# Kernel optimization log

Measured on AMD Instinct MI355X. Metric: run time of the kernel, lower is better.

Reference implementation:

```python
import jax, jax.numpy as jnp
import numpy as np

TEMPERATURE = 0.2
NUMBER_CLASSES = 1000
LOSS_SCALE = 0.001

N, F = 8192, 256
M = 20000
DEPTH = 4


def setup_inputs() -> dict:
    key = jax.random.key(0)
    k1, k2, k3, k4 = jax.random.split(key, 4)
    gt_labels = jax.random.randint(k1, (N,), 0, NUMBER_CLASSES, dtype=jnp.int32)
    box_features = jax.random.normal(k2, (N, F), dtype=jnp.float32)
    memory = jax.random.normal(k3, (M, F), dtype=jnp.float32)
    trace_idx = jax.random.randint(k4, (NUMBER_CLASSES, DEPTH), 0, M, dtype=jnp.int32)
    return {"gt_labels": gt_labels, "box_features": box_features,
            "memory": memory, "trace_idx": trace_idx}


def reference(gt_labels, box_features, memory, trace_idx):
    # logits[i, j] = dot(f_i, m_j) / T  (the nested python loops fused into one GEMM)
    logits = jnp.einsum('nf,mf->nm', box_features, memory) / TEMPERATURE  # [N, M]
    # fenmu = sum_j exp(logits)  ->  log(fenmu) = logsumexp
    lse = jax.nn.logsumexp(logits, axis=-1)  # [N]
    # gather the trace entries for each item's label: [N, DEPTH]
    traces = trace_idx[gt_labels]  # [N, DEPTH]
    sel = jnp.take_along_axis(logits, traces, axis=1)  # [N, DEPTH]
    depth_w = jnp.arange(DEPTH, dtype=logits.dtype)  # gj = depth
    sum_gj = depth_w.sum()  # sum of layer weights (0+1+2+3)
    # per item: -sum_d gj * log(sim_d / fenmu) / sum_gj
    per_item = -jnp.sum((sel - lse[:, None]) * depth_w, axis=-1) / sum_gj  # [N]
    # background filter: items with label == number_classes contribute nothing
    fg = (gt_labels != NUMBER_CLASSES)
    loss = jnp.sum(jnp.where(fg, per_item, 0.0)) * LOSS_SCALE
    return loss
```

## Files before the change

kernel.cpp:

```cpp
#include <hip/hip_runtime.h>
#include <hip/hip_bf16.h>
#include <stdint.h>

#define NROWS 8192
#define FDIM 256
#define MCOLS 20000
#define NT32 625
#define MSPLIT 16
#define NCLS 1000
#define LOG2E 1.44269504088896f
#define LN2   0.69314718055994f


typedef short short8 __attribute__((ext_vector_type(8)));
typedef float f32x16 __attribute__((ext_vector_type(16)));

typedef __attribute__((address_space(3))) unsigned int lds_u32;
typedef const __attribute__((address_space(1))) unsigned int glb_u32;

__device__ __forceinline__ float ex2(float x) {
    float r;
    asm("v_exp_f32 %0, %1" : "=v"(r) : "v"(x));
    return r;
}

__device__ __forceinline__ unsigned short f2bf(float x) {
    unsigned u = __float_as_uint(x);
    unsigned r = (u + 0x7FFFu + ((u >> 16) & 1u)) >> 16;
    return (unsigned short)r;
}

__global__ void conv_kernel(const float* __restrict__ in, unsigned short* __restrict__ out,
                            int n4, float scale) {
    int idx = blockIdx.x * blockDim.x + threadIdx.x;
    if (idx >= n4) return;
    float4 v = ((const float4*)in)[idx];
    ushort4 o;
    o.x = f2bf(v.x * scale); o.y = f2bf(v.y * scale);
    o.z = f2bf(v.z * scale); o.w = f2bf(v.w * scale);
    ((ushort4*)out)[idx] = o;
}

__global__ void sel_kernel(const int* __restrict__ gt, const float* __restrict__ F,
                           const float* __restrict__ Mem, const int* __restrict__ trace,
                           float* __restrict__ wsel) {
    int lane = threadIdx.x & 63, wid = threadIdx.x >> 6;
    int i = blockIdx.x * 4 + wid;
    int label = gt[i];
    float w = 0.0f;
    if (label >= 0 && label < NCLS) {
        float4 fv = ((const float4*)(F + (size_t)i * FDIM))[lane];
        #pragma unroll
        for (int d = 1; d <= 3; ++d) {
            int tr = trace[label * 4 + d];
            float4 mv = ((const float4*)(Mem + (size_t)tr * FDIM))[lane];
            float dot = fv.x*mv.x + fv.y*mv.y + fv.z*mv.z + fv.w*mv.w;
            #pragma unroll
            for (int off = 32; off >= 1; off >>= 1) dot += __shfl_xor(dot, off, 64);
            w += (float)d * dot;
        }
    }
    if (lane == 0) wsel[i] = w * 5.0f;
}

__global__ __launch_bounds__(256, 2) void lse_gemm(
        const unsigned short* __restrict__ Fb, const unsigned short* __restrict__ Mb,
        float* __restrict__ pm, float* __restrict__ ps) {
    __shared__ __align__(16) char smem[2 * 16384];

    const int split  = blockIdx.x;
    const int rowblk = blockIdx.y;
    const int tid  = threadIdx.x;
    const int lane = tid & 63, wid = tid >> 6;
    const int r0 = lane & 31;
    const int hi = lane >> 5;
    const int rowbase = rowblk * 128 + wid * 32;

    short8 a[16];
    #pragma unroll
    for (int kk = 0; kk < 16; ++kk)
        a[kk] = *(const short8*)(Fb + (size_t)(rowbase + r0) * FDIM + kk * 16 + hi * 8);

    float m = -3.0e38f, s = 0.0f;

    const int t0 = (split * NT32) / MSPLIT;
    const int t1 = ((split + 1) * NT32) / MSPLIT;

    int srcoff[4];
    #pragma unroll
    for (int c = 0; c < 4; ++c) {
        const int g = (wid * 4 + c) * 64 + lane;
        const int j = g >> 5, o = g & 31;
        srcoff[c] = j * 512 + ((o ^ j) << 4);
    }

#define STAGE(BUF, t)                                                              \
    do {                                                                           \
        const char* srcT = (const char*)Mb + (size_t)(t) * 16384;                  \
        _Pragma("unroll")                                                          \
        for (int c = 0; c < 4; ++c) {                                              \
            __builtin_amdgcn_global_load_lds(                                      \
                (glb_u32*)(srcT + srcoff[c]),                                      \
                (lds_u32*)(smem + (BUF) * 16384 + (wid * 4 + c) * 1024),           \
                16, 0, 0);                                                         \
        }                                                                          \
    } while (0)

    int roff[16];
    #pragma unroll
    for (int kk = 0; kk < 16; ++kk)
        roff[kk] = r0 * 512 + ((((kk << 1) | hi) ^ r0) << 4);

#define BODYC(BUF)                                                                 \
    do {                                                                           \
        f32x16 acc = {0,0,0,0,0,0,0,0,0,0,0,0,0,0,0,0};                            \
        __builtin_amdgcn_s_setprio(1);                                             \
        _Pragma("unroll")                                                          \
        for (int kk = 0; kk < 16; ++kk) {                                          \
            short8 b = *(const short8*)(smem + (BUF) * 16384 + roff[kk]);          \
            acc = __builtin_amdgcn_mfma_f32_32x32x16_bf16(b, a[kk], acc, 0, 0, 0); \
        }                                                                          \
        __builtin_amdgcn_s_setprio(0);                                             \
        float x0 = fmaxf(fmaxf(acc[0],  acc[1]),  acc[2]);                         \
        float x1 = fmaxf(fmaxf(acc[3],  acc[4]),  acc[5]);                         \
        float x2 = fmaxf(fmaxf(acc[6],  acc[7]),  acc[8]);                         \
        float x3 = fmaxf(fmaxf(acc[9],  acc[10]), acc[11]);                        \
        float x4 = fmaxf(fmaxf(acc[12], acc[13]), acc[14]);                        \
        float x5 = fmaxf(fmaxf(x0, x1), x2);                                       \
        float x6 = fmaxf(fmaxf(x3, x4), acc[15]);                                  \
        float nm = fmaxf(fmaxf(x5, x6), m);                                        \
        float p0 = 0.f, p1 = 0.f, p2 = 0.f, p3 = 0.f;                              \
        _Pragma("unroll")                                                          \
        for (int i = 0; i < 16; i += 4) {                                          \
            p0 += ex2(acc[i]     - nm); p1 += ex2(acc[i + 1] - nm);                \
            p2 += ex2(acc[i + 2] - nm); p3 += ex2(acc[i + 3] - nm);                \
        }                                                                          \
        s = fmaf(s, ex2(m - nm), (p0 + p1) + (p2 + p3));                           \
        m = nm;                                                                    \
    } while (0)

    STAGE(0, t0);
    __syncthreads();

    int t = t0;
    while (t + 2 <= t1) {
        STAGE(1, t + 1);
        BODYC(0);
        __syncthreads();
        if (t + 2 < t1) STAGE(0, t + 2);
        BODYC(1);
        __syncthreads();
        t += 2;
    }
    if (t < t1) BODYC(0);

#undef BODYC
#undef STAGE

    {
        float om = __shfl_xor(m, 32, 64);
        float os = __shfl_xor(s, 32, 64);
        float nm = fmaxf(m, om);
        float sf = fmaf(s, ex2(m - nm), os * ex2(om - nm));
        if (lane < 32) {
            pm[split * NROWS + rowbase + lane] = nm;
            ps[split * NROWS + rowbase + lane] = sf;
        }
    }
}

__global__ void finalize_kernel(const int* __restrict__ gt, const float* __restrict__ wsel,
                                const float* __restrict__ pm, const float* __restrict__ ps,
                                float* __restrict__ bpart) {
    int tid = threadIdx.x;
    int i = blockIdx.x * 256 + tid;
    float mv[MSPLIT];
    float M = -3.0e38f;
    #pragma unroll
    for (int k = 0; k < MSPLIT; ++k) { mv[k] = pm[k * NROWS + i]; M = fmaxf(M, mv[k]); }
    float S = 0.0f;
    #pragma unroll
    for (int k = 0; k < MSPLIT; ++k) S += ps[k * NROWS + i] * ex2(mv[k] - M);
    float lse = (M + __log2f(S)) * LN2;
    int label = gt[i];
    float per = (label >= 0 && label < NCLS) ? (lse - wsel[i] * (1.0f / 6.0f)) : 0.0f;
    #pragma unroll
    for (int off = 32; off >= 1; off >>= 1) per += __shfl_xor(per, off, 64);
    __shared__ float red[4];
    int lane = tid & 63, wid = tid >> 6;
    if (lane == 0) red[wid] = per;
    __syncthreads();
    if (tid == 0) bpart[blockIdx.x] = red[0] + red[1] + red[2] + red[3];
}

__global__ void sum_kernel(const float* __restrict__ bpart, float* __restrict__ out) {
    int tid = threadIdx.x;
    float v = (tid < 32) ? bpart[tid] : 0.0f;
    #pragma unroll
    for (int off = 32; off >= 1; off >>= 1) v += __shfl_xor(v, off, 64);
    if (tid == 0) out[0] = 0.001f * v;
}

extern "C" void kernel_launch(void* const* d_in, const int* in_sizes, int n_in,
                              void* d_out, int out_size, void* d_ws, size_t ws_size,
                              hipStream_t stream) {
    const int*   gt    = (const int*)d_in[0];
    const float* F     = (const float*)d_in[1];
    const float* Mem   = (const float*)d_in[2];
    const int*   trace = (const int*)d_in[3];
    float* out = (float*)d_out;

    char* w = (char*)d_ws;
    unsigned short* Mb = (unsigned short*)w;
    unsigned short* Fb = (unsigned short*)(w + 10240000);
    float* wsel  = (float*)(w + 14434304);
    float* pm    = (float*)(w + 14467072);
    float* ps    = (float*)(w + 14991360);
    float* bpart = (float*)(w + 15515648);

    conv_kernel<<<dim3((MCOLS * FDIM / 4) / 256), dim3(256), 0, stream>>>(Mem, Mb, MCOLS * FDIM / 4, 1.0f);
    conv_kernel<<<dim3((NROWS * FDIM / 4) / 256), dim3(256), 0, stream>>>(F, Fb, NROWS * FDIM / 4, 5.0f * LOG2E);
    sel_kernel<<<dim3(NROWS / 4), dim3(256), 0, stream>>>(gt, F, Mem, trace, wsel);
    lse_gemm<<<dim3(MSPLIT, NROWS / 128), dim3(256), 0, stream>>>(Fb, Mb, pm, ps);
    finalize_kernel<<<dim3(NROWS / 256), dim3(256), 0, stream>>>(gt, wsel, pm, ps, bpart);
    sum_kernel<<<dim3(1), dim3(64), 0, stream>>>(bpart, out);
}
```

Measured before the change: 109.2 us.

## Process two memory tiles per pipeline stage with dual MFMA accumulators

Result: slower. 112.1 us (+2.7%).

```diff
diff --git a/kernel.cpp b/kernel.cpp
--- a/kernel.cpp
+++ b/kernel.cpp
@@ -28,6 +28,17 @@
     unsigned u = __float_as_uint(x);
     unsigned r = (u + 0x7FFFu + ((u >> 16) & 1u)) >> 16;
     return (unsigned short)r;
+}
+
+__device__ __forceinline__ float vmax16(f32x16 v) {
+    float x0 = fmaxf(fmaxf(v[0],  v[1]),  v[2]);
+    float x1 = fmaxf(fmaxf(v[3],  v[4]),  v[5]);
+    float x2 = fmaxf(fmaxf(v[6],  v[7]),  v[8]);
+    float x3 = fmaxf(fmaxf(v[9],  v[10]), v[11]);
+    float x4 = fmaxf(fmaxf(v[12], v[13]), v[14]);
+    float x5 = fmaxf(fmaxf(x0, x1), x2);
+    float x6 = fmaxf(fmaxf(x3, x4), v[15]);
+    return fmaxf(x5, x6);
 }
 
 __global__ void conv_kernel(const float* __restrict__ in, unsigned short* __restrict__ out,
@@ -66,7 +77,7 @@
 __global__ __launch_bounds__(256, 2) void lse_gemm(
         const unsigned short* __restrict__ Fb, const unsigned short* __restrict__ Mb,
         float* __restrict__ pm, float* __restrict__ ps) {
-    __shared__ __align__(16) char smem[2 * 16384];
+    __shared__ __align__(16) char smem[2 * 32768];
 
     const int split  = blockIdx.x;
     const int rowblk = blockIdx.y;
@@ -86,49 +97,103 @@
     const int t0 = (split * NT32) / MSPLIT;
     const int t1 = ((split + 1) * NT32) / MSPLIT;
 
-    int srcoff[4];
+    int srcoff[8];
+    #pragma unroll
+    for (int c = 0; c < 8; ++c) {
+        const int g  = (wid * 8 + c) * 64 + lane;
+        const int st = g >> 10;
+        const int gs = g & 1023;
+        const int j = gs >> 5, o = gs & 31;
+        srcoff[c] = st * 16384 + j * 512 + ((o ^ j) << 4);
+    }
+
+#define STAGE2(BUF, t)                                                             \
+    do {                                                                           \
+        const char* srcT = (const char*)Mb + (size_t)(t) * 16384;                  \
+        _Pragma("unroll")                                                          \
+        for (int c = 0; c < 8; ++c) {                                              \
+            __builtin_amdgcn_global_load_lds(                                      \
+                (glb_u32*)(srcT + srcoff[c]),                                      \
+                (lds_u32*)(smem + (BUF) * 32768 + (wid * 8 + c) * 1024),           \
+                16, 0, 0);                                                         \
+        }                                                                          \
+    } while (0)
+
+#define STAGE1(BUF, t)                                                             \
+    do {                                                                           \
+        const char* srcT = (const char*)Mb + (size_t)(t) * 16384;                  \
+        _Pragma("unroll")                                                          \
+        for (int c = 0; c < 4; ++c) {                                              \
+            __builtin_amdgcn_global_load_lds(                                      \
+                (glb_u32*)(srcT + srcoff[c]),                                      \
+                (lds_u32*)(smem + (BUF) * 32768 + (wid * 4 + c) * 1024),           \
+                16, 0, 0);                                                         \
+        }                                                                          \
+    } while (0)
+
+    int roff[16];
+    #pragma unroll
+    for (int kk = 0; kk < 16; ++kk)
+        roff[kk] = r0 * 512 + ((((kk << 1) | hi) ^ r0) << 4);
+
+    int srcoff1[4];
     #pragma unroll
     for (int c = 0; c < 4; ++c) {
         const int g = (wid * 4 + c) * 64 + lane;
         const int j = g >> 5, o = g & 31;
-        srcoff[c] = j * 512 + ((o ^ j) << 4);
-    }
-
-#define STAGE(BUF, t)                                                              \
+        srcoff1[c] = j * 512 + ((o ^ j) << 4);
+    }
+#undef STAGE1
+#define STAGE1(BUF, t)                                                             \
     do {                                                                           \
         const char* srcT = (const char*)Mb + (size_t)(t) * 16384;                  \
         _Pragma("unroll")                                                          \
         for (int c = 0; c < 4; ++c) {                                              \
             __builtin_amdgcn_global_load_lds(                                      \
-                (glb_u32*)(srcT + srcoff[c]),                                      \
-                (lds_u32*)(smem + (BUF) * 16384 + (wid * 4 + c) * 1024),           \
+                (glb_u32*)(srcT + srcoff1[c]),                                     \
+                (lds_u32*)(smem + (BUF) * 32768 + (wid * 4 + c) * 1024),           \
                 16, 0, 0);                                                         \
         }                                                                          \
     } while (0)
 
-    int roff[16];
-    #pragma unroll
-    for (int kk = 0; kk < 16; ++kk)
-        roff[kk] = r0 * 512 + ((((kk << 1) | hi) ^ r0) << 4);
-
-#define BODYC(BUF)                                                                 \
+#define BODY2(BUF)                                                                 \
+    do {                                                                           \
+        f32x16 acc0 = {0,0,0,0,0,0,0,0,0,0,0,0,0,0,0,0};                           \
+        f32x16 acc1 = {0,0,0,0,0,0,0,0,0,0,0,0,0,0,0,0};                           \
+        __builtin_amdgcn_s_setprio(1);                                             \
+        _Pragma("unroll")                                                          \
+        for (int kk = 0; kk < 16; ++kk) {                                          \
+            const char* bp = smem + (BUF) * 32768 + roff[kk];                      \
+            short8 b0 = *(const short8*)bp;                                        \
+            short8 b1 = *(const short8*)(bp + 16384);                              \
+            acc0 = __builtin_amdgcn_mfma_f32_32x32x16_bf16(b0, a[kk], acc0, 0, 0, 0); \
+            acc1 = __builtin_amdgcn_mfma_f32_32x32x16_bf16(b1, a[kk], acc1, 0, 0, 0); \
+        }                                                                          \
+        __builtin_amdgcn_s_setprio(0);                                             \
+        float nm = fmaxf(m, fmaxf(vmax16(acc0), vmax16(acc1)));                    \
+        float p0 = 0.f, p1 = 0.f, p2 = 0.f, p3 = 0.f;                              \
+        _Pragma("unroll")                                                          \
+        for (int i = 0; i < 16; i += 4) {                                          \
+            p0 += ex2(acc0[i]     - nm); p1 += ex2(acc0[i + 1] - nm);              \
+            p2 += ex2(acc0[i + 2] - nm); p3 += ex2(acc0[i + 3] - nm);              \
+            p0 += ex2(acc1[i]     - nm); p1 += ex2(acc1[i + 1] - nm);              \
+            p2 += ex2(acc1[i + 2] - nm); p3 += ex2(acc1[i + 3] - nm);              \
+        }                                                                          \
+        s = fmaf(s, ex2(m - nm), (p0 + p1) + (p2 + p3));                           \
+        m = nm;                                                                    \
+    } while (0)
+
+#define BODY1(BUF)                                                                 \
     do {                                                                           \
         f32x16 acc = {0,0,0,0,0,0,0,0,0,0,0,0,0,0,0,0};                            \
         __builtin_amdgcn_s_setprio(1);                                             \
         _Pragma("unroll")                                                          \
         for (int kk = 0; kk < 16; ++kk) {                                          \
-            short8 b = *(const short8*)(smem + (BUF) * 16384 + roff[kk]);          \
+            short8 b = *(const short8*)(smem + (BUF) * 32768 + roff[kk]);          \
             acc = __builtin_amdgcn_mfma_f32_32x32x16_bf16(b, a[kk], acc, 0, 0, 0); \
         }                                                                          \
         __builtin_amdgcn_s_setprio(0);                                             \
-        float x0 = fmaxf(fmaxf(acc[0],  acc[1]),  acc[2]);                         \
-        float x1 = fmaxf(fmaxf(acc[3],  acc[4]),  acc[5]);                         \
-        float x2 = fmaxf(fmaxf(acc[6],  acc[7]),  acc[8]);                         \
-        float x3 = fmaxf(fmaxf(acc[9],  acc[10]), acc[11]);                        \
-        float x4 = fmaxf(fmaxf(acc[12], acc[13]), acc[14]);                        \
-        float x5 = fmaxf(fmaxf(x0, x1), x2);                                       \
-        float x6 = fmaxf(fmaxf(x3, x4), acc[15]);                                  \
-        float nm = fmaxf(fmaxf(x5, x6), m);                                        \
+        float nm = fmaxf(vmax16(acc), m);                                          \
         float p0 = 0.f, p1 = 0.f, p2 = 0.f, p3 = 0.f;                              \
         _Pragma("unroll")                                                          \
         for (int i = 0; i < 16; i += 4) {                                          \
@@ -139,23 +204,35 @@
         m = nm;                                                                    \
     } while (0)
 
-    STAGE(0, t0);
+    const int P = (t1 - t0) >> 1;
+    const int T = (t1 - t0) & 1;
+
+    STAGE2(0, t0);
     __syncthreads();
 
-    int t = t0;
-    while (t + 2 <= t1) {
-        STAGE(1, t + 1);
-        BODYC(0);
+    int t = t0, p = 0;
+    while (p + 2 <= P) {
+        STAGE2(1, t + 2);
+        BODY2(0);
         __syncthreads();
-        if (t + 2 < t1) STAGE(0, t + 2);
-        BODYC(1);
+        if (p + 3 <= P)              STAGE2(0, t + 4);
+        else if (p + 2 == P && T)    STAGE1(0, t + 4);
+        BODY2(1);
         __syncthreads();
-        t += 2;
-    }
-    if (t < t1) BODYC(0);
-
-#undef BODYC
-#undef STAGE
+        t += 4; p += 2;
+    }
+    if (p < P) {
+        if (T) STAGE1(1, t + 2);
+        BODY2(0);
+        if (T) { __syncthreads(); BODY1(1); }
+    } else if (T) {
+        BODY1(0);
+    }
+
+#undef BODY1
+#undef BODY2
+#undef STAGE1
+#undef STAGE2
 
     {
         float om = __shfl_xor(m, 32, 64);
```

## Double rows per wave so each LDS B fragment feeds two MFMAs

Applied to the files above, without the earlier changes.

After: 118.3 us. 8.4% more time.

```diff
diff --git a/kernel.cpp b/kernel.cpp
--- a/kernel.cpp
+++ b/kernel.cpp
@@ -28,6 +28,17 @@
     unsigned u = __float_as_uint(x);
     unsigned r = (u + 0x7FFFu + ((u >> 16) & 1u)) >> 16;
     return (unsigned short)r;
+}
+
+__device__ __forceinline__ float vmax16(f32x16 v) {
+    float x0 = fmaxf(fmaxf(v[0],  v[1]),  v[2]);
+    float x1 = fmaxf(fmaxf(v[3],  v[4]),  v[5]);
+    float x2 = fmaxf(fmaxf(v[6],  v[7]),  v[8]);
+    float x3 = fmaxf(fmaxf(v[9],  v[10]), v[11]);
+    float x4 = fmaxf(fmaxf(v[12], v[13]), v[14]);
+    float x5 = fmaxf(fmaxf(x0, x1), x2);
+    float x6 = fmaxf(fmaxf(x3, x4), v[15]);
+    return fmaxf(x5, x6);
 }
 
 __global__ void conv_kernel(const float* __restrict__ in, unsigned short* __restrict__ out,
@@ -74,14 +85,21 @@
     const int lane = tid & 63, wid = tid >> 6;
     const int r0 = lane & 31;
     const int hi = lane >> 5;
-    const int rowbase = rowblk * 128 + wid * 32;
-
-    short8 a[16];
-    #pragma unroll
-    for (int kk = 0; kk < 16; ++kk)
-        a[kk] = *(const short8*)(Fb + (size_t)(rowbase + r0) * FDIM + kk * 16 + hi * 8);
-
-    float m = -3.0e38f, s = 0.0f;
+    const int rowbase = rowblk * 256 + wid * 64;
+
+    short8 al[16], ah[16];
+    #pragma unroll
+    for (int kk = 0; kk < 16; ++kk) {
+        al[kk] = *(const short8*)(Fb + (size_t)(rowbase + r0)      * FDIM + kk * 16 + hi * 8);
+        ah[kk] = *(const short8*)(Fb + (size_t)(rowbase + 32 + r0) * FDIM + kk * 16 + hi * 8);
+    }
+    #pragma unroll
+    for (int kk = 0; kk < 16; ++kk) {
+        asm volatile("" : "+v"(al[kk]));
+        asm volatile("" : "+a"(ah[kk]));
+    }
+
+    float m0 = -3.0e38f, s0 = 0.0f, m1 = -3.0e38f, s1 = 0.0f;
 
     const int t0 = (split * NT32) / MSPLIT;
     const int t1 = ((split + 1) * NT32) / MSPLIT;
@@ -113,30 +131,38 @@
 
 #define BODYC(BUF)                                                                 \
     do {                                                                           \
-        f32x16 acc = {0,0,0,0,0,0,0,0,0,0,0,0,0,0,0,0};                            \
+        f32x16 acc0 = {0,0,0,0,0,0,0,0,0,0,0,0,0,0,0,0};                           \
+        f32x16 acc1 = {0,0,0,0,0,0,0,0,0,0,0,0,0,0,0,0};                           \
         __builtin_amdgcn_s_setprio(1);                                             \
         _Pragma("unroll")                                                          \
         for (int kk = 0; kk < 16; ++kk) {                                          \
             short8 b = *(const short8*)(smem + (BUF) * 16384 + roff[kk]);          \
-            acc = __builtin_amdgcn_mfma_f32_32x32x16_bf16(b, a[kk], acc, 0, 0, 0); \
+            acc0 = __builtin_amdgcn_mfma_f32_32x32x16_bf16(b, al[kk], acc0, 0, 0, 0); \
+            acc1 = __builtin_amdgcn_mfma_f32_32x32x16_bf16(b, ah[kk], acc1, 0, 0, 0); \
         }                                                                          \
         __builtin_amdgcn_s_setprio(0);                                             \
-        float x0 = fmaxf(fmaxf(acc[0],  acc[1]),  acc[2]);                         \
-        float x1 = fmaxf(fmaxf(acc[3],  acc[4]),  acc[5]);                         \
-        float x2 = fmaxf(fmaxf(acc[6],  acc[7]),  acc[8]);                         \
-        float x3 = fmaxf(fmaxf(acc[9],  acc[10]), acc[11]);                        \
-        float x4 = fmaxf(fmaxf(acc[12], acc[13]), acc[14]);                        \
-        float x5 = fmaxf(fmaxf(x0, x1), x2);                                       \
-        float x6 = fmaxf(fmaxf(x3, x4), acc[15]);                                  \
-        float nm = fmaxf(fmaxf(x5, x6), m);                                        \
-        float p0 = 0.f, p1 = 0.f, p2 = 0.f, p3 = 0.f;                              \
-        _Pragma("unroll")                                                          \
-        for (int i = 0; i < 16; i += 4) {                                          \
-            p0 += ex2(acc[i]     - nm); p1 += ex2(acc[i + 1] - nm);                \
-            p2 += ex2(acc[i + 2] - nm); p3 += ex2(acc[i + 3] - nm);                \
-        }                                                                          \
-        s = fmaf(s, ex2(m - nm), (p0 + p1) + (p2 + p3));                           \
-        m = nm;                                                                    \
+        {                                                                          \
+            float nm = fmaxf(vmax16(acc0), m0);                                    \
+            float p0 = 0.f, p1 = 0.f, p2 = 0.f, p3 = 0.f;                          \
+            _Pragma("unroll")                                                      \
+            for (int i = 0; i < 16; i += 4) {                                      \
+                p0 += ex2(acc0[i]     - nm); p1 += ex2(acc0[i + 1] - nm);          \
+                p2 += ex2(acc0[i + 2] - nm); p3 += ex2(acc0[i + 3] - nm);          \
+            }                                                                      \
+            s0 = fmaf(s0, ex2(m0 - nm), (p0 + p1) + (p2 + p3));                    \
+            m0 = nm;                                                               \
+        }                                                                          \
+        {                                                                          \
+            float nm = fmaxf(vmax16(acc1), m1);                                    \
+            float p0 = 0.f, p1 = 0.f, p2 = 0.f, p3 = 0.f;                          \
+            _Pragma("unroll")                                                      \
+            for (int i = 0; i < 16; i += 4) {                                      \
+                p0 += ex2(acc1[i]     - nm); p1 += ex2(acc1[i + 1] - nm);          \
+                p2 += ex2(acc1[i + 2] - nm); p3 += ex2(acc1[i + 3] - nm);          \
+            }                                                                      \
+            s1 = fmaf(s1, ex2(m1 - nm), (p0 + p1) + (p2 + p3));                    \
+            m1 = nm;                                                               \
+        }                                                                          \
     } while (0)
 
     STAGE(0, t0);
@@ -158,13 +184,23 @@
 #undef STAGE
 
     {
-        float om = __shfl_xor(m, 32, 64);
-        float os = __shfl_xor(s, 32, 64);
-        float nm = fmaxf(m, om);
-        float sf = fmaf(s, ex2(m - nm), os * ex2(om - nm));
+        float om = __shfl_xor(m0, 32, 64);
+        float os = __shfl_xor(s0, 32, 64);
+        float nm = fmaxf(m0, om);
+        float sf = fmaf(s0, ex2(m0 - nm), os * ex2(om - nm));
         if (lane < 32) {
             pm[split * NROWS + rowbase + lane] = nm;
             ps[split * NROWS + rowbase + lane] = sf;
+        }
+    }
+    {
+        float om = __shfl_xor(m1, 32, 64);
+        float os = __shfl_xor(s1, 32, 64);
+        float nm = fmaxf(m1, om);
+        float sf = fmaf(s1, ex2(m1 - nm), os * ex2(om - nm));
+        if (lane < 32) {
+            pm[split * NROWS + rowbase + 32 + lane] = nm;
+            ps[split * NROWS + rowbase + 32 + lane] = sf;
         }
     }
 }
@@ -221,7 +257,7 @@
     conv_kernel<<<dim3((MCOLS * FDIM / 4) / 256), dim3(256), 0, stream>>>(Mem, Mb, MCOLS * FDIM / 4, 1.0f);
     conv_kernel<<<dim3((NROWS * FDIM / 4) / 256), dim3(256), 0, stream>>>(F, Fb, NROWS * FDIM / 4, 5.0f * LOG2E);
     sel_kernel<<<dim3(NROWS / 4), dim3(256), 0, stream>>>(gt, F, Mem, trace, wsel);
-    lse_gemm<<<dim3(MSPLIT, NROWS / 128), dim3(256), 0, stream>>>(Fb, Mb, pm, ps);
+    lse_gemm<<<dim3(MSPLIT, NROWS / 256), dim3(256), 0, stream>>>(Fb, Mb, pm, ps);
     finalize_kernel<<<dim3(NROWS / 256), dim3(256), 0, stream>>>(gt, wsel, pm, ps, bpart);
     sum_kernel<<<dim3(1), dim3(64), 0, stream>>>(bpart, out);
 }
```

## Pre-swizzle memory bank into MFMA fragment order, raise GEMM occupancy

Applied to the files above, without the earlier changes.

Measured after the change: 109.4 us. No clear change (+0.3%).

```diff
diff --git a/kernel.cpp b/kernel.cpp
--- a/kernel.cpp
+++ b/kernel.cpp
@@ -28,6 +28,17 @@
     unsigned u = __float_as_uint(x);
     unsigned r = (u + 0x7FFFu + ((u >> 16) & 1u)) >> 16;
     return (unsigned short)r;
+}
+
+__device__ __forceinline__ float vmax16(f32x16 v) {
+    float x0 = fmaxf(fmaxf(v[0],  v[1]),  v[2]);
+    float x1 = fmaxf(fmaxf(v[3],  v[4]),  v[5]);
+    float x2 = fmaxf(fmaxf(v[6],  v[7]),  v[8]);
+    float x3 = fmaxf(fmaxf(v[9],  v[10]), v[11]);
+    float x4 = fmaxf(fmaxf(v[12], v[13]), v[14]);
+    float x5 = fmaxf(fmaxf(x0, x1), x2);
+    float x6 = fmaxf(fmaxf(x3, x4), v[15]);
+    return fmaxf(x5, x6);
 }
 
 __global__ void conv_kernel(const float* __restrict__ in, unsigned short* __restrict__ out,
@@ -39,6 +50,20 @@
     o.x = f2bf(v.x * scale); o.y = f2bf(v.y * scale);
     o.z = f2bf(v.z * scale); o.w = f2bf(v.w * scale);
     ((ushort4*)out)[idx] = o;
+}
+
+__global__ void conv_mb2(const float* __restrict__ in, unsigned short* __restrict__ out) {
+    int g = blockIdx.x * 256 + threadIdx.x;
+    int s = g & 63, kk = (g >> 6) & 15, t = g >> 10;
+    const float* src = in + (size_t)(t * 32 + (s & 31)) * FDIM + kk * 16 + (s >> 5) * 8;
+    float4 v0 = ((const float4*)src)[0];
+    float4 v1 = ((const float4*)src)[1];
+    short8 w;
+    w[0] = (short)f2bf(v0.x); w[1] = (short)f2bf(v0.y);
+    w[2] = (short)f2bf(v0.z); w[3] = (short)f2bf(v0.w);
+    w[4] = (short)f2bf(v1.x); w[5] = (short)f2bf(v1.y);
+    w[6] = (short)f2bf(v1.z); w[7] = (short)f2bf(v1.w);
+    *(short8*)(out + (size_t)g * 8) = w;
 }
 
 __global__ void sel_kernel(const int* __restrict__ gt, const float* __restrict__ F,
@@ -63,8 +88,8 @@
     if (lane == 0) wsel[i] = w * 5.0f;
 }
 
-__global__ __launch_bounds__(256, 2) void lse_gemm(
-        const unsigned short* __restrict__ Fb, const unsigned short* __restrict__ Mb,
+__global__ __launch_bounds__(256, 4) void lse_gemm(
+        const unsigned short* __restrict__ Fb, const unsigned short* __restrict__ Mb2,
         float* __restrict__ pm, float* __restrict__ ps) {
     __shared__ __align__(16) char smem[2 * 16384];
 
@@ -75,6 +100,7 @@
     const int r0 = lane & 31;
     const int hi = lane >> 5;
     const int rowbase = rowblk * 128 + wid * 32;
+    const int l16 = lane << 4;
 
     short8 a[16];
     #pragma unroll
@@ -86,49 +112,30 @@
     const int t0 = (split * NT32) / MSPLIT;
     const int t1 = ((split + 1) * NT32) / MSPLIT;
 
-    int srcoff[4];
-    #pragma unroll
-    for (int c = 0; c < 4; ++c) {
-        const int g = (wid * 4 + c) * 64 + lane;
-        const int j = g >> 5, o = g & 31;
-        srcoff[c] = j * 512 + ((o ^ j) << 4);
-    }
-
 #define STAGE(BUF, t)                                                              \
     do {                                                                           \
-        const char* srcT = (const char*)Mb + (size_t)(t) * 16384;                  \
+        const char* srcT = (const char*)Mb2 + (size_t)(t) * 16384 + l16;           \
         _Pragma("unroll")                                                          \
         for (int c = 0; c < 4; ++c) {                                              \
             __builtin_amdgcn_global_load_lds(                                      \
-                (glb_u32*)(srcT + srcoff[c]),                                      \
+                (glb_u32*)(srcT + (wid * 4 + c) * 1024),                           \
                 (lds_u32*)(smem + (BUF) * 16384 + (wid * 4 + c) * 1024),           \
                 16, 0, 0);                                                         \
         }                                                                          \
     } while (0)
 
-    int roff[16];
-    #pragma unroll
-    for (int kk = 0; kk < 16; ++kk)
-        roff[kk] = r0 * 512 + ((((kk << 1) | hi) ^ r0) << 4);
-
 #define BODYC(BUF)                                                                 \
     do {                                                                           \
+        const char* bp = smem + (BUF) * 16384 + l16;                               \
         f32x16 acc = {0,0,0,0,0,0,0,0,0,0,0,0,0,0,0,0};                            \
         __builtin_amdgcn_s_setprio(1);                                             \
         _Pragma("unroll")                                                          \
         for (int kk = 0; kk < 16; ++kk) {                                          \
-            short8 b = *(const short8*)(smem + (BUF) * 16384 + roff[kk]);          \
+            short8 b = *(const short8*)(bp + kk * 1024);                           \
             acc = __builtin_amdgcn_mfma_f32_32x32x16_bf16(b, a[kk], acc, 0, 0, 0); \
         }                                                                          \
         __builtin_amdgcn_s_setprio(0);                                             \
-        float x0 = fmaxf(fmaxf(acc[0],  acc[1]),  acc[2]);                         \
-        float x1 = fmaxf(fmaxf(acc[3],  acc[4]),  acc[5]);                         \
-        float x2 = fmaxf(fmaxf(acc[6],  acc[7]),  acc[8]);                         \
-        float x3 = fmaxf(fmaxf(acc[9],  acc[10]), acc[11]);                        \
-        float x4 = fmaxf(fmaxf(acc[12], acc[13]), acc[14]);                        \
-        float x5 = fmaxf(fmaxf(x0, x1), x2);                                       \
-        float x6 = fmaxf(fmaxf(x3, x4), acc[15]);                                  \
-        float nm = fmaxf(fmaxf(x5, x6), m);                                        \
+        float nm = fmaxf(vmax16(acc), m);                                          \
         float p0 = 0.f, p1 = 0.f, p2 = 0.f, p3 = 0.f;                              \
         _Pragma("unroll")                                                          \
         for (int i = 0; i < 16; i += 4) {                                          \
@@ -211,17 +218,17 @@
     float* out = (float*)d_out;
 
     char* w = (char*)d_ws;
-    unsigned short* Mb = (unsigned short*)w;
-    unsigned short* Fb = (unsigned short*)(w + 10240000);
+    unsigned short* Mb2 = (unsigned short*)w;
+    unsigned short* Fb  = (unsigned short*)(w + 10240000);
     float* wsel  = (float*)(w + 14434304);
     float* pm    = (float*)(w + 14467072);
     float* ps    = (float*)(w + 14991360);
     float* bpart = (float*)(w + 15515648);
 
-    conv_kernel<<<dim3((MCOLS * FDIM / 4) / 256), dim3(256), 0, stream>>>(Mem, Mb, MCOLS * FDIM / 4, 1.0f);
+    conv_mb2<<<dim3(2500), dim3(256), 0, stream>>>(Mem, Mb2);
     conv_kernel<<<dim3((NROWS * FDIM / 4) / 256), dim3(256), 0, stream>>>(F, Fb, NROWS * FDIM / 4, 5.0f * LOG2E);
     sel_kernel<<<dim3(NROWS / 4), dim3(256), 0, stream>>>(gt, F, Mem, trace, wsel);
-    lse_gemm<<<dim3(MSPLIT, NROWS / 128), dim3(256), 0, stream>>>(Fb, Mb, pm, ps);
+    lse_gemm<<<dim3(MSPLIT, NROWS / 128), dim3(256), 0, stream>>>(Fb, Mb2, pm, ps);
     finalize_kernel<<<dim3(NROWS / 256), dim3(256), 0, stream>>>(gt, wsel, pm, ps, bpart);
     sum_kernel<<<dim3(1), dim3(64), 0, stream>>>(bpart, out);
 }
```
